# Kernel optimization log

Measured on AMD Instinct MI355X. Metric: run time of the kernel, lower is better.

## Reference

```python
import jax, jax.numpy as jnp
import numpy as np

B, S, H = 2, 2048, 1024
NH, DH = 16, 64  # num heads, head dim

def setup_inputs() -> dict:
    key = jax.random.key(0)
    ks = jax.random.split(key, 4)
    scale = 0.02
    return {
        "hidden_states": jax.random.normal(ks[0], (B, S, H), dtype=jnp.float32),
        "attention_mask": jnp.zeros((B, 1, 1, S), dtype=jnp.float32),  # additive mask
        "Wq": jax.random.normal(ks[1], (H, H), dtype=jnp.float32) * scale,
        "bq": jnp.zeros((H,), dtype=jnp.float32),
        "Wk": jax.random.normal(ks[2], (H, H), dtype=jnp.float32) * scale,
        "bk": jnp.zeros((H,), dtype=jnp.float32),
        "Wv": jax.random.normal(ks[3], (H, H), dtype=jnp.float32) * scale,
        "bv": jnp.zeros((H,), dtype=jnp.float32),
    }

def _split_heads(x):
    # [B,S,H] -> [B,NH,S,DH]
    return x.reshape(B, S, NH, DH).transpose(0, 2, 1, 3)

def reference(hidden_states, attention_mask, Wq, bq, Wk, bk, Wv, bv):
    q = _split_heads(hidden_states @ Wq + bq)
    k = _split_heads(hidden_states @ Wk + bk)
    v = _split_heads(hidden_states @ Wv + bv)
    # scores: [B,NH,S,S]
    scores = jnp.einsum('bhqd,bhkd->bhqk', q, k) / jnp.asarray(np.sqrt(DH), scores_dtype := q.dtype)
    scores = scores + attention_mask  # additive mask broadcast
    probs = jax.nn.softmax(scores, axis=-1)
    out = jnp.einsum('bhqk,bhkd->bhqd', probs, v)  # [B,NH,S,DH]
    out = out.transpose(0, 2, 1, 3).reshape(B, S, H)
    return out
```

## Files before the change

kernel.cpp:

```cpp
#include <hip/hip_runtime.h>
#include <hip/hip_bf16.h>

#define Bn  2
#define Sn  2048
#define Hn  1024
#define NHn 16
#define DHn 64
#define Mn  (Bn * Sn)

typedef __attribute__((ext_vector_type(4)))  float    f32x4;
typedef __attribute__((ext_vector_type(16))) float    f32x16;
typedef __attribute__((ext_vector_type(8)))  _Float16 h8;
typedef __attribute__((ext_vector_type(4)))  _Float16 h4;
typedef __attribute__((ext_vector_type(2)))  __fp16   fp16v2;

#define MFMA16F(a, b, c) __builtin_amdgcn_mfma_f32_16x16x32_f16(a, b, c, 0, 0, 0)
#define MFMA32F(a, b, c) __builtin_amdgcn_mfma_f32_32x32x16_f16(a, b, c, 0, 0, 0)

__device__ __forceinline__ void glds16(const void* g, void* l) {
    __builtin_amdgcn_global_load_lds(
        (const __attribute__((address_space(1))) unsigned int*)g,
        (__attribute__((address_space(3))) unsigned int*)l, 16, 0, 0);
}

__device__ __forceinline__ unsigned pkrtz(float a, float b) {
    union { fp16v2 h; unsigned u; } c;
    c.h = __builtin_amdgcn_cvt_pkrtz(a, b);
    return c.u;
}

__global__ __launch_bounds__(256) void cvt_x(
    const float* __restrict__ X, _Float16* __restrict__ Xh)
{
    const int i = blockIdx.x * 256 + threadIdx.x;
    float4 x = ((const float4*)X)[i];
    h4 o;
    o[0] = (_Float16)x.x; o[1] = (_Float16)x.y;
    o[2] = (_Float16)x.z; o[3] = (_Float16)x.w;
    *(h4*)&Xh[(size_t)i * 4] = o;
}

__global__ __launch_bounds__(256) void cvt_mask(
    const float* __restrict__ mask, float* __restrict__ mask2)
{
    const int i = blockIdx.x * 256 + threadIdx.x;
    mask2[i] = mask[i] * 1.44269504f;
}

__global__ __launch_bounds__(256) void cvt_wT(
    const float* __restrict__ W0, const float* __restrict__ W1,
    const float* __restrict__ W2, _Float16* __restrict__ WT)
{
    const int which = blockIdx.z;
    const float* W = (which == 0) ? W0 : (which == 1 ? W1 : W2);
    _Float16* O = WT + (size_t)which * Hn * Hn;

    const int k0 = blockIdx.x * 64;
    const int n0 = blockIdx.y * 64;
    const int tid = threadIdx.x;

    __shared__ float Ws[64][65];

#pragma unroll
    for (int it = 0; it < 4; ++it) {
        const int idx = tid + 256 * it;
        const int row = idx >> 4, c4 = (idx & 15) * 4;
        float4 w = *(const float4*)&W[(size_t)(k0 + row) * Hn + n0 + c4];
        Ws[row][c4 + 0] = w.x; Ws[row][c4 + 1] = w.y;
        Ws[row][c4 + 2] = w.z; Ws[row][c4 + 3] = w.w;
    }
    __syncthreads();
#pragma unroll
    for (int it = 0; it < 16; ++it) {
        const int e = tid + 256 * it;
        const int k = e & 63, n = e >> 6;
        O[(size_t)(n0 + n) * Hn + k0 + k] = (_Float16)Ws[k][n];
    }
}

__global__ __launch_bounds__(256) void qkv_mfma(
    const _Float16* __restrict__ Xh, const _Float16* __restrict__ WTA,
    const float* __restrict__ b0, const float* __restrict__ b1,
    const float* __restrict__ b2,
    _Float16* __restrict__ Qh, _Float16* __restrict__ Kh,
    _Float16* __restrict__ VTh)
{
    const int which = blockIdx.z;
    const _Float16* WT = WTA + (size_t)which * Hn * Hn;
    const float* bias = (which == 0) ? b0 : (which == 1 ? b1 : b2);
    _Float16* Dst = (which == 0) ? Qh : (which == 1 ? Kh : VTh);

    const int m0 = blockIdx.x * 128;
    const int n0 = blockIdx.y * 128;
    const int tid  = threadIdx.x;
    const int wid  = tid >> 6;
    const int lane = tid & 63;
    const int l16  = lane & 15;
    const int quad = lane >> 4;
    const int wm = wid >> 1, wn = wid & 1;

    __shared__ _Float16 Ah[128 * 32], Bh[128 * 32];

    f32x4 acc[4][4];
#pragma unroll
    for (int i = 0; i < 4; ++i)
#pragma unroll
        for (int j = 0; j < 4; ++j) acc[i][j] = (f32x4){0.f, 0.f, 0.f, 0.f};

    for (int kt = 0; kt < Hn / 32; ++kt) {
        const int k0 = kt * 32;
        __syncthreads();
#pragma unroll
        for (int c = 0; c < 2; ++c) {
            const int idx = (wid * 2 + c) * 64 + lane;
            const int row = idx >> 2;
            const int cg  = (idx & 3) ^ (row & 3);
            glds16(&Xh[(size_t)(m0 + row) * Hn + k0 + cg * 8],
                   &Ah[(wid * 2 + c) * 512]);
            glds16(&WT[(size_t)(n0 + row) * Hn + k0 + cg * 8],
                   &Bh[(wid * 2 + c) * 512]);
        }
        __syncthreads();

        h8 xa[4], wb[4];
#pragma unroll
        for (int t = 0; t < 4; ++t) {
            const int ar = wm * 64 + t * 16 + l16;
            const int br = wn * 64 + t * 16 + l16;
            xa[t] = *(const h8*)&Ah[ar * 32 + ((quad ^ (ar & 3)) * 8)];
            wb[t] = *(const h8*)&Bh[br * 32 + ((quad ^ (br & 3)) * 8)];
        }
        if (which < 2) {
#pragma unroll
            for (int i = 0; i < 4; ++i)
#pragma unroll
                for (int j = 0; j < 4; ++j)
                    acc[i][j] = MFMA16F(xa[i], wb[j], acc[i][j]);
        } else {
#pragma unroll
            for (int i = 0; i < 4; ++i)
#pragma unroll
                for (int j = 0; j < 4; ++j)
                    acc[i][j] = MFMA16F(wb[i], xa[j], acc[i][j]);
        }
    }

    if (which < 2) {
#pragma unroll
        for (int j = 0; j < 4; ++j) {
            const int n = n0 + wn * 64 + j * 16 + l16;
            const float bv = bias[n];
            const int hh = n >> 6, dd = n & 63;
#pragma unroll
            for (int i = 0; i < 4; ++i) {
                const int mb = m0 + wm * 64 + i * 16 + quad * 4;
#pragma unroll
                for (int r = 0; r < 4; ++r) {
                    const int m = mb + r;
                    const int b = m >> 11, s = m & (Sn - 1);
                    Dst[(((size_t)b * NHn + hh) * Sn + s) * DHn + dd] =
                        (_Float16)(acc[i][j][r] + bv);
                }
            }
        }
    } else {
#pragma unroll
        for (int i = 0; i < 4; ++i) {
#pragma unroll
            for (int r = 0; r < 4; ++r) {
                const int n = n0 + wn * 64 + i * 16 + quad * 4 + r;
                const float bv = bias[n];
                const int hh = n >> 6, dd = n & 63;
#pragma unroll
                for (int j = 0; j < 4; ++j) {
                    const int m = m0 + wm * 64 + j * 16 + l16;
                    const int b = m >> 11, s = m & (Sn - 1);
                    Dst[(((size_t)b * NHn + hh) * DHn + dd) * Sn + s] =
                        (_Float16)(acc[i][j][r] + bv);
                }
            }
        }
    }
}

#define SCALE_LOG2E 0.180336880f

__global__ __launch_bounds__(256) void attn(
    const _Float16* __restrict__ Qh, const _Float16* __restrict__ Kh,
    const _Float16* __restrict__ VTh, const float* __restrict__ mask2,
    float* __restrict__ Out)
{
    const int qb = blockIdx.x;
    const int h  = blockIdx.y;
    const int b  = blockIdx.z;
    const int bh = b * NHn + h;

    const int tid  = threadIdx.x;
    const int wid  = tid >> 6;
    const int lane = tid & 63;
    const int l32  = lane & 31;
    const int hi   = lane >> 5;

    __shared__ _Float16 Kb[2][4096];
    __shared__ _Float16 Vb[2][4096];
    __shared__ float MskAll[Sn];
    __shared__ float Ilds[4][32];

    const int q0 = qb * 128 + wid * 32;
    const size_t qbase = ((size_t)bh * Sn + q0 + l32) * DHn;
    h8 qf[4];
#pragma unroll
    for (int kd = 0; kd < 4; ++kd)
        qf[kd] = *(const h8*)&Qh[qbase + kd * 16 + hi * 8];

    {
        const float4* msrc = (const float4*)(mask2 + (size_t)b * Sn);
#pragma unroll
        for (int i = 0; i < 2; ++i) {
            const int idx = tid + 256 * i;
            *(float4*)&MskAll[idx * 4] = msrc[idx];
        }
    }

    f32x16 o[2];
#pragma unroll
    for (int dt = 0; dt < 2; ++dt) o[dt] = (f32x16)(0.f);
    float l_lane = 0.f;

    const int idx0 = (wid * 2 + 0) * 64 + lane;
    const int idx1 = (wid * 2 + 1) * 64 + lane;
    const int row0 = idx0 >> 3, cg0 = (idx0 & 7) ^ (row0 & 7);
    const int row1 = idx1 >> 3, cg1 = (idx1 & 7) ^ (row1 & 7);
    const _Float16* kp0 = Kh  + (size_t)bh * Sn * DHn + (size_t)row0 * DHn + cg0 * 8;
    const _Float16* kp1 = Kh  + (size_t)bh * Sn * DHn + (size_t)row1 * DHn + cg1 * 8;
    const _Float16* vp0 = VTh + (size_t)bh * DHn * Sn + (size_t)row0 * Sn + cg0 * 8;
    const _Float16* vp1 = VTh + (size_t)bh * DHn * Sn + (size_t)row1 * Sn + cg1 * 8;
    _Float16* KbP = &Kb[0][0];
    _Float16* VbP = &Vb[0][0];
    const int ld0 = (wid * 2 + 0) * 512;
    const int ld1 = (wid * 2 + 1) * 512;

    glds16(kp0, KbP + ld0);  glds16(kp1, KbP + ld1);
    glds16(vp0, VbP + ld0);  glds16(vp1, VbP + ld1);
    kp0 += 64 * DHn; kp1 += 64 * DHn; vp0 += 64; vp1 += 64;

    for (int kt = 0; kt < Sn / 64; ++kt) {
        const int cur = kt & 1;
        __syncthreads();

        if (kt + 1 < Sn / 64) {
            const int nb = (cur ^ 1) * 4096;
            glds16(kp0, KbP + nb + ld0);  glds16(kp1, KbP + nb + ld1);
            glds16(vp0, VbP + nb + ld0);  glds16(vp1, VbP + nb + ld1);
            kp0 += 64 * DHn; kp1 += 64 * DHn; vp0 += 64; vp1 += 64;
        }
        const _Float16* Kc = KbP + cur * 4096;
        const _Float16* Vc = VbP + cur * 4096;

#pragma unroll
        for (int t = 0; t < 2; ++t) {
            f32x16 s = (f32x16)(0.f);
#pragma unroll
            for (int kd = 0; kd < 4; ++kd) {
                const int row = t * 32 + l32;
                h8 kf = *(const h8*)&Kc[row * 64 + (((kd * 2 + hi) ^ (row & 7)) * 8)];
                s = MFMA32F(kf, qf[kd], s);
            }

            unsigned pk[4][2];
#pragma unroll
            for (int g2 = 0; g2 < 4; ++g2) {
                float4 mv = *(const float4*)&MskAll[kt * 64 + t * 32 + g2 * 8 + hi * 4];
                float p0 = __builtin_amdgcn_exp2f(s[g2 * 4 + 0] * SCALE_LOG2E + mv.x);
                float p1 = __builtin_amdgcn_exp2f(s[g2 * 4 + 1] * SCALE_LOG2E + mv.y);
                float p2 = __builtin_amdgcn_exp2f(s[g2 * 4 + 2] * SCALE_LOG2E + mv.z);
                float p3 = __builtin_amdgcn_exp2f(s[g2 * 4 + 3] * SCALE_LOG2E + mv.w);
                l_lane += (p0 + p1) + (p2 + p3);
                pk[g2][0] = pkrtz(p0, p1);
                pk[g2][1] = pkrtz(p2, p3);
            }

            unsigned sx = hi ? pk[0][0] : pk[1][0];
            unsigned sy = hi ? pk[0][1] : pk[1][1];
            unsigned rx = __shfl_xor(sx, 32);
            unsigned ry = __shfl_xor(sy, 32);
            union { unsigned u[4]; h8 v; } af0;
            if (hi == 0) { af0.u[0] = pk[0][0]; af0.u[1] = pk[0][1]; af0.u[2] = rx; af0.u[3] = ry; }
            else         { af0.u[0] = rx;       af0.u[1] = ry;       af0.u[2] = pk[1][0]; af0.u[3] = pk[1][1]; }

            unsigned sx2 = hi ? pk[2][0] : pk[3][0];
            unsigned sy2 = hi ? pk[2][1] : pk[3][1];
            unsigned rx2 = __shfl_xor(sx2, 32);
            unsigned ry2 = __shfl_xor(sy2, 32);
            union { unsigned u[4]; h8 v; } af1;
            if (hi == 0) { af1.u[0] = pk[2][0]; af1.u[1] = pk[2][1]; af1.u[2] = rx2; af1.u[3] = ry2; }
            else         { af1.u[0] = rx2;      af1.u[1] = ry2;      af1.u[2] = pk[3][0]; af1.u[3] = pk[3][1]; }

#pragma unroll
            for (int dt = 0; dt < 2; ++dt) {
                const int row = dt * 32 + l32;
                h8 vf0 = *(const h8*)&Vc[row * 64 + (((t * 4 + hi)     ^ (row & 7)) * 8)];
                o[dt] = MFMA32F(af0.v, vf0, o[dt]);
                h8 vf1 = *(const h8*)&Vc[row * 64 + (((t * 4 + 2 + hi) ^ (row & 7)) * 8)];
                o[dt] = MFMA32F(af1.v, vf1, o[dt]);
            }
        }
    }

    const float l_tot = l_lane + __shfl_xor(l_lane, 32);
    if (lane < 32) Ilds[wid][l32] = 1.0f / l_tot;

#pragma unroll
    for (int g2 = 0; g2 < 4; ++g2) {
        float4 iv = *(const float4*)&Ilds[wid][hi * 4 + g2 * 8];
#pragma unroll
        for (int e = 0; e < 4; ++e) {
            const int r = g2 * 4 + e;
            const int q = q0 + 4 * hi + 8 * g2 + e;
            const size_t ob = ((size_t)b * Sn + q) * Hn + h * DHn;
            const float sc = ((const float*)&iv)[e];
#pragma unroll
            for (int dt = 0; dt < 2; ++dt)
                Out[ob + dt * 32 + l32] = o[dt][r] * sc;
        }
    }
}

extern "C" void kernel_launch(void* const* d_in, const int* in_sizes, int n_in,
                              void* d_out, int out_size, void* d_ws, size_t ws_size,
                              hipStream_t stream) {
    const float* X    = (const float*)d_in[0];
    const float* mask = (const float*)d_in[1];
    const float* Wq   = (const float*)d_in[2];
    const float* bq   = (const float*)d_in[3];
    const float* Wk   = (const float*)d_in[4];
    const float* bk   = (const float*)d_in[5];
    const float* Wv   = (const float*)d_in[6];
    const float* bv   = (const float*)d_in[7];
    float* out = (float*)d_out;

    const size_t NE = (size_t)Mn * Hn;
    _Float16* Xh  = (_Float16*)d_ws;
    _Float16* WT  = Xh + NE;
    _Float16* Qh  = WT + (size_t)3 * Hn * Hn;
    _Float16* Kh  = Qh + NE;
    _Float16* VTh = Kh + NE;
    float*    m2  = (float*)(VTh + NE);

    cvt_x<<<dim3(Mn * Hn / 1024), dim3(256), 0, stream>>>(X, Xh);
    cvt_mask<<<dim3(Bn * Sn / 256), dim3(256), 0, stream>>>(mask, m2);
    cvt_wT<<<dim3(16, 16, 3), dim3(256), 0, stream>>>(Wq, Wk, Wv, WT);

    dim3 g1(Mn / 128, Hn / 128, 3), b1(256);
    qkv_mfma<<<g1, b1, 0, stream>>>(Xh, WT, bq, bk, bv, Qh, Kh, VTh);

    dim3 g2(Sn / 128, NHn, Bn), b2(256);
    attn<<<g2, b2, 0, stream>>>(Qh, Kh, VTh, m2, out);
}
```

Baseline: 198.0 us.

## Double-buffer QKV GEMM tiles and process two query subtiles per attention warp

The QKV projection GEMM now double-buffers its LDS tiles and prefetches the next K-slice while computing the current one, which removes one barrier per iteration. The attention kernel gives each warp 64 queries instead of 32, so every K and V fragment read from LDS is reused for two query subtiles, and the grid is halved. Register pressure goes up because of two sets of accumulators and Q fragments, and launch_bounds(256,1) is added. With only 256 attention blocks, occupancy and load balance across CUs may suffer.

```diff
diff --git a/kernel.cpp b/kernel.cpp
--- a/kernel.cpp
+++ b/kernel.cpp
@@ -99,7 +99,7 @@
     const int quad = lane >> 4;
     const int wm = wid >> 1, wn = wid & 1;
 
-    __shared__ _Float16 Ah[128 * 32], Bh[128 * 32];
+    __shared__ _Float16 Ah[2][4096], Bh[2][4096];
 
     f32x4 acc[4][4];
 #pragma unroll
@@ -107,28 +107,39 @@
 #pragma unroll
         for (int j = 0; j < 4; ++j) acc[i][j] = (f32x4){0.f, 0.f, 0.f, 0.f};
 
+    const int idxc0 = (wid * 2 + 0) * 64 + lane;
+    const int idxc1 = (wid * 2 + 1) * 64 + lane;
+    const int arow0 = idxc0 >> 2, acg0 = ((idxc0 & 3) ^ (arow0 & 3));
+    const int arow1 = idxc1 >> 2, acg1 = ((idxc1 & 3) ^ (arow1 & 3));
+    const _Float16* pA0 = Xh + (size_t)(m0 + arow0) * Hn + acg0 * 8;
+    const _Float16* pA1 = Xh + (size_t)(m0 + arow1) * Hn + acg1 * 8;
+    const _Float16* pB0 = WT + (size_t)(n0 + arow0) * Hn + acg0 * 8;
+    const _Float16* pB1 = WT + (size_t)(n0 + arow1) * Hn + acg1 * 8;
+    const int ld0 = (wid * 2 + 0) * 512;
+    const int ld1 = (wid * 2 + 1) * 512;
+
+    glds16(pA0, &Ah[0][ld0]);  glds16(pA1, &Ah[0][ld1]);
+    glds16(pB0, &Bh[0][ld0]);  glds16(pB1, &Bh[0][ld1]);
+    pA0 += 32; pA1 += 32; pB0 += 32; pB1 += 32;
+
     for (int kt = 0; kt < Hn / 32; ++kt) {
-        const int k0 = kt * 32;
+        const int cur = kt & 1;
         __syncthreads();
-#pragma unroll
-        for (int c = 0; c < 2; ++c) {
-            const int idx = (wid * 2 + c) * 64 + lane;
-            const int row = idx >> 2;
-            const int cg  = (idx & 3) ^ (row & 3);
-            glds16(&Xh[(size_t)(m0 + row) * Hn + k0 + cg * 8],
-                   &Ah[(wid * 2 + c) * 512]);
-            glds16(&WT[(size_t)(n0 + row) * Hn + k0 + cg * 8],
-                   &Bh[(wid * 2 + c) * 512]);
-        }
-        __syncthreads();
+
+        if (kt + 1 < Hn / 32) {
+            const int nxt = cur ^ 1;
+            glds16(pA0, &Ah[nxt][ld0]);  glds16(pA1, &Ah[nxt][ld1]);
+            glds16(pB0, &Bh[nxt][ld0]);  glds16(pB1, &Bh[nxt][ld1]);
+            pA0 += 32; pA1 += 32; pB0 += 32; pB1 += 32;
+        }
 
         h8 xa[4], wb[4];
 #pragma unroll
         for (int t = 0; t < 4; ++t) {
             const int ar = wm * 64 + t * 16 + l16;
             const int br = wn * 64 + t * 16 + l16;
-            xa[t] = *(const h8*)&Ah[ar * 32 + ((quad ^ (ar & 3)) * 8)];
-            wb[t] = *(const h8*)&Bh[br * 32 + ((quad ^ (br & 3)) * 8)];
+            xa[t] = *(const h8*)&Ah[cur][ar * 32 + ((quad ^ (ar & 3)) * 8)];
+            wb[t] = *(const h8*)&Bh[cur][br * 32 + ((quad ^ (br & 3)) * 8)];
         }
         if (which < 2) {
 #pragma unroll
@@ -185,7 +196,7 @@
 
 #define SCALE_LOG2E 0.180336880f
 
-__global__ __launch_bounds__(256) void attn(
+__global__ __launch_bounds__(256, 1) void attn(
     const _Float16* __restrict__ Qh, const _Float16* __restrict__ Kh,
     const _Float16* __restrict__ VTh, const float* __restrict__ mask2,
     float* __restrict__ Out)
@@ -204,14 +215,17 @@
     __shared__ _Float16 Kb[2][4096];
     __shared__ _Float16 Vb[2][4096];
     __shared__ float MskAll[Sn];
-    __shared__ float Ilds[4][32];
-
-    const int q0 = qb * 128 + wid * 32;
-    const size_t qbase = ((size_t)bh * Sn + q0 + l32) * DHn;
-    h8 qf[4];
-#pragma unroll
-    for (int kd = 0; kd < 4; ++kd)
-        qf[kd] = *(const h8*)&Qh[qbase + kd * 16 + hi * 8];
+    __shared__ float Ilds[4][64];
+
+    const int q0w = qb * 256 + wid * 64;
+    h8 qf[2][4];
+#pragma unroll
+    for (int qs = 0; qs < 2; ++qs) {
+        const size_t qbase = ((size_t)bh * Sn + q0w + qs * 32 + l32) * DHn;
+#pragma unroll
+        for (int kd = 0; kd < 4; ++kd)
+            qf[qs][kd] = *(const h8*)&Qh[qbase + kd * 16 + hi * 8];
+    }
 
     {
         const float4* msrc = (const float4*)(mask2 + (size_t)b * Sn);
@@ -222,10 +236,12 @@
         }
     }
 
-    f32x16 o[2];
-#pragma unroll
-    for (int dt = 0; dt < 2; ++dt) o[dt] = (f32x16)(0.f);
-    float l_lane = 0.f;
+    f32x16 o[2][2];
+#pragma unroll
+    for (int qs = 0; qs < 2; ++qs)
+#pragma unroll
+        for (int dt = 0; dt < 2; ++dt) o[qs][dt] = (f32x16)(0.f);
+    float l_lane[2] = {0.f, 0.f};
 
     const int idx0 = (wid * 2 + 0) * 64 + lane;
     const int idx1 = (wid * 2 + 1) * 64 + lane;
@@ -259,69 +275,91 @@
 
 #pragma unroll
         for (int t = 0; t < 2; ++t) {
-            f32x16 s = (f32x16)(0.f);
-#pragma unroll
-            for (int kd = 0; kd < 4; ++kd) {
-                const int row = t * 32 + l32;
-                h8 kf = *(const h8*)&Kc[row * 64 + (((kd * 2 + hi) ^ (row & 7)) * 8)];
-                s = MFMA32F(kf, qf[kd], s);
-            }
-
-            unsigned pk[4][2];
-#pragma unroll
-            for (int g2 = 0; g2 < 4; ++g2) {
-                float4 mv = *(const float4*)&MskAll[kt * 64 + t * 32 + g2 * 8 + hi * 4];
-                float p0 = __builtin_amdgcn_exp2f(s[g2 * 4 + 0] * SCALE_LOG2E + mv.x);
-                float p1 = __builtin_amdgcn_exp2f(s[g2 * 4 + 1] * SCALE_LOG2E + mv.y);
-                float p2 = __builtin_amdgcn_exp2f(s[g2 * 4 + 2] * SCALE_LOG2E + mv.z);
-                float p3 = __builtin_amdgcn_exp2f(s[g2 * 4 + 3] * SCALE_LOG2E + mv.w);
-                l_lane += (p0 + p1) + (p2 + p3);
-                pk[g2][0] = pkrtz(p0, p1);
-                pk[g2][1] = pkrtz(p2, p3);
-            }
-
-            unsigned sx = hi ? pk[0][0] : pk[1][0];
-            unsigned sy = hi ? pk[0][1] : pk[1][1];
-            unsigned rx = __shfl_xor(sx, 32);
-            unsigned ry = __shfl_xor(sy, 32);
-            union { unsigned u[4]; h8 v; } af0;
-            if (hi == 0) { af0.u[0] = pk[0][0]; af0.u[1] = pk[0][1]; af0.u[2] = rx; af0.u[3] = ry; }
-            else         { af0.u[0] = rx;       af0.u[1] = ry;       af0.u[2] = pk[1][0]; af0.u[3] = pk[1][1]; }
-
-            unsigned sx2 = hi ? pk[2][0] : pk[3][0];
-            unsigned sy2 = hi ? pk[2][1] : pk[3][1];
-            unsigned rx2 = __shfl_xor(sx2, 32);
-            unsigned ry2 = __shfl_xor(sy2, 32);
-            union { unsigned u[4]; h8 v; } af1;
-            if (hi == 0) { af1.u[0] = pk[2][0]; af1.u[1] = pk[2][1]; af1.u[2] = rx2; af1.u[3] = ry2; }
-            else         { af1.u[0] = rx2;      af1.u[1] = ry2;      af1.u[2] = pk[3][0]; af1.u[3] = pk[3][1]; }
-
+            const int krow = t * 32 + l32;
+            h8 kf[4];
+#pragma unroll
+            for (int kd = 0; kd < 4; ++kd)
+                kf[kd] = *(const h8*)&Kc[krow * 64 + (((kd * 2 + hi) ^ (krow & 7)) * 8)];
+
+            f32x16 s[2];
+#pragma unroll
+            for (int qs = 0; qs < 2; ++qs) {
+                f32x16 c = (f32x16)(0.f);
+#pragma unroll
+                for (int kd = 0; kd < 4; ++kd)
+                    c = MFMA32F(kf[kd], qf[qs][kd], c);
+                s[qs] = c;
+            }
+
+            h8 vf0[2], vf1[2];
 #pragma unroll
             for (int dt = 0; dt < 2; ++dt) {
-                const int row = dt * 32 + l32;
-                h8 vf0 = *(const h8*)&Vc[row * 64 + (((t * 4 + hi)     ^ (row & 7)) * 8)];
-                o[dt] = MFMA32F(af0.v, vf0, o[dt]);
-                h8 vf1 = *(const h8*)&Vc[row * 64 + (((t * 4 + 2 + hi) ^ (row & 7)) * 8)];
-                o[dt] = MFMA32F(af1.v, vf1, o[dt]);
-            }
-        }
-    }
-
-    const float l_tot = l_lane + __shfl_xor(l_lane, 32);
-    if (lane < 32) Ilds[wid][l32] = 1.0f / l_tot;
-
-#pragma unroll
-    for (int g2 = 0; g2 < 4; ++g2) {
-        float4 iv = *(const float4*)&Ilds[wid][hi * 4 + g2 * 8];
-#pragma unroll
-        for (int e = 0; e < 4; ++e) {
-            const int r = g2 * 4 + e;
-            const int q = q0 + 4 * hi + 8 * g2 + e;
-            const size_t ob = ((size_t)b * Sn + q) * Hn + h * DHn;
-            const float sc = ((const float*)&iv)[e];
-#pragma unroll
-            for (int dt = 0; dt < 2; ++dt)
-                Out[ob + dt * 32 + l32] = o[dt][r] * sc;
+                const int vrow = dt * 32 + l32;
+                vf0[dt] = *(const h8*)&Vc[vrow * 64 + (((t * 4 + hi)     ^ (vrow & 7)) * 8)];
+                vf1[dt] = *(const h8*)&Vc[vrow * 64 + (((t * 4 + 2 + hi) ^ (vrow & 7)) * 8)];
+            }
+
+#pragma unroll
+            for (int qs = 0; qs < 2; ++qs) {
+                unsigned pk[4][2];
+#pragma unroll
+                for (int g2 = 0; g2 < 4; ++g2) {
+                    float4 mv = *(const float4*)&MskAll[kt * 64 + t * 32 + g2 * 8 + hi * 4];
+                    float p0 = __builtin_amdgcn_exp2f(s[qs][g2 * 4 + 0] * SCALE_LOG2E + mv.x);
+                    float p1 = __builtin_amdgcn_exp2f(s[qs][g2 * 4 + 1] * SCALE_LOG2E + mv.y);
+                    float p2 = __builtin_amdgcn_exp2f(s[qs][g2 * 4 + 2] * SCALE_LOG2E + mv.z);
+                    float p3 = __builtin_amdgcn_exp2f(s[qs][g2 * 4 + 3] * SCALE_LOG2E + mv.w);
+                    l_lane[qs] += (p0 + p1) + (p2 + p3);
+                    pk[g2][0] = pkrtz(p0, p1);
+                    pk[g2][1] = pkrtz(p2, p3);
+                }
+
+                unsigned sx = hi ? pk[0][0] : pk[1][0];
+                unsigned sy = hi ? pk[0][1] : pk[1][1];
+                unsigned rx = __shfl_xor(sx, 32);
+                unsigned ry = __shfl_xor(sy, 32);
+                union { unsigned u[4]; h8 v; } af0;
+                if (hi == 0) { af0.u[0] = pk[0][0]; af0.u[1] = pk[0][1]; af0.u[2] = rx; af0.u[3] = ry; }
+                else         { af0.u[0] = rx;       af0.u[1] = ry;       af0.u[2] = pk[1][0]; af0.u[3] = pk[1][1]; }
+
+                unsigned sx2 = hi ? pk[2][0] : pk[3][0];
+                unsigned sy2 = hi ? pk[2][1] : pk[3][1];
+                unsigned rx2 = __shfl_xor(sx2, 32);
+                unsigned ry2 = __shfl_xor(sy2, 32);
+                union { unsigned u[4]; h8 v; } af1;
+                if (hi == 0) { af1.u[0] = pk[2][0]; af1.u[1] = pk[2][1]; af1.u[2] = rx2; af1.u[3] = ry2; }
+                else         { af1.u[0] = rx2;      af1.u[1] = ry2;      af1.u[2] = pk[3][0]; af1.u[3] = pk[3][1]; }
+
+#pragma unroll
+                for (int dt = 0; dt < 2; ++dt) {
+                    o[qs][dt] = MFMA32F(af0.v, vf0[dt], o[qs][dt]);
+                    o[qs][dt] = MFMA32F(af1.v, vf1[dt], o[qs][dt]);
+                }
+            }
+        }
+    }
+
+#pragma unroll
+    for (int qs = 0; qs < 2; ++qs) {
+        const float l_tot = l_lane[qs] + __shfl_xor(l_lane[qs], 32);
+        if (lane < 32) Ilds[wid][qs * 32 + l32] = 1.0f / l_tot;
+    }
+
+#pragma unroll
+    for (int qs = 0; qs < 2; ++qs) {
+#pragma unroll
+        for (int g2 = 0; g2 < 4; ++g2) {
+            float4 iv = *(const float4*)&Ilds[wid][qs * 32 + hi * 4 + g2 * 8];
+#pragma unroll
+            for (int e = 0; e < 4; ++e) {
+                const int r = g2 * 4 + e;
+                const int q = q0w + qs * 32 + 4 * hi + 8 * g2 + e;
+                const size_t ob = ((size_t)b * Sn + q) * Hn + h * DHn;
+                const float sc = ((const float*)&iv)[e];
+#pragma unroll
+                for (int dt = 0; dt < 2; ++dt)
+                    Out[ob + dt * 32 + l32] = o[qs][dt][r] * sc;
+            }
         }
     }
 }
@@ -354,6 +392,6 @@
     dim3 g1(Mn / 128, Hn / 128, 3), b1(256);
     qkv_mfma<<<g1, b1, 0, stream>>>(Xh, WT, bq, bk, bv, Qh, Kh, VTh);
 
-    dim3 g2(Sn / 128, NHn, Bn), b2(256);
+    dim3 g2(Sn / 256, NHn, Bn), b2(256);
     attn<<<g2, b2, 0, stream>>>(Qh, Kh, VTh, m2, out);
 }
```

Measured after the change: 209.6 us. 5.8% more time.
